# Kernel tuning notes

Hardware: AMD Instinct MI355X
Metric: run time of the kernel (lower is better)

Reference implementation:

```python
import jax, jax.numpy as jnp
import numpy as np

B, H, S, D = 2, 16, 2048, 64


def setup_inputs() -> dict:
    key = jax.random.key(0)
    kq, kk, kv = jax.random.split(key, 3)
    Q = jax.random.normal(kq, (B, H, S, D), dtype=jnp.float32)
    K = jax.random.normal(kk, (B, H, S, D), dtype=jnp.float32)
    V = jax.random.normal(kv, (B, H, S, D), dtype=jnp.float32)
    # causal mask, broadcastable over batch/heads; True = attend
    mask = jnp.tril(jnp.ones((S, S), dtype=bool))[None, None, :, :]
    return {"Q": Q, "K": K, "V": V, "mask": mask}


def reference(Q, K, V, mask):
    d_k = Q.shape[-1]
    # [b,h,s_q,s_k] scores
    scores = jnp.einsum("bhqd,bhkd->bhqk", Q, K) / jnp.sqrt(jnp.float32(d_k))
    scores = jnp.where(mask, scores, -jnp.inf)
    attn = jax.nn.softmax(scores, axis=-1)
    out = jnp.einsum("bhqk,bhkd->bhqd", attn, V)
    return out
```

## Files before the change

kernel.cpp:

```cpp
#include <hip/hip_runtime.h>

#define SDIM 2048
#define DDIM 64
#define BHN  32

using f32x4  = __attribute__((ext_vector_type(4))) float;
using f32x16 = __attribute__((ext_vector_type(16))) float;
using bf16x8 = __attribute__((ext_vector_type(8))) __bf16;
using s16x8  = __attribute__((ext_vector_type(8))) short;

union FragU { s16x8 s; bf16x8 b; uint4 u4; };
union US8   { unsigned short u[8]; uint4 v; };
union PW    { __bf16 h[2]; unsigned int u; };

__device__ __forceinline__ unsigned short f2bf(float f) {
    unsigned int u = __builtin_bit_cast(unsigned int, f);
    u += 0x7fffu + ((u >> 16) & 1u);
    return (unsigned short)(u >> 16);
}

__device__ __forceinline__ unsigned int packbf(float a, float b) {
    PW w; w.h[0] = (__bf16)a; w.h[1] = (__bf16)b; return w.u;
}

__device__ __forceinline__ float fexp2(float x) { return __builtin_amdgcn_exp2f(x); }

__device__ __forceinline__ void gload16(const void* g, void* l) {
    __builtin_amdgcn_global_load_lds(
        (const __attribute__((address_space(1))) void*)g,
        (__attribute__((address_space(3))) void*)l, 16, 0, 0);
}

__global__ __launch_bounds__(256) void conv_fused_kernel(
    const float* __restrict__ K, const float* __restrict__ V,
    unsigned short* __restrict__ Kb, unsigned short* __restrict__ Vt)
{
    const int s0 = blockIdx.x * 64;
    const int bh = blockIdx.y;
    const int t  = threadIdx.x;

    {
        const size_t off = ((size_t)bh * SDIM + s0) * DDIM;
        const float4* src = (const float4*)(K + off);
        float4 a = src[t*4+0], b = src[t*4+1], c = src[t*4+2], d = src[t*4+3];
        US8 o0, o1;
        o0.u[0]=f2bf(a.x); o0.u[1]=f2bf(a.y); o0.u[2]=f2bf(a.z); o0.u[3]=f2bf(a.w);
        o0.u[4]=f2bf(b.x); o0.u[5]=f2bf(b.y); o0.u[6]=f2bf(b.z); o0.u[7]=f2bf(b.w);
        o1.u[0]=f2bf(c.x); o1.u[1]=f2bf(c.y); o1.u[2]=f2bf(c.z); o1.u[3]=f2bf(c.w);
        o1.u[4]=f2bf(d.x); o1.u[5]=f2bf(d.y); o1.u[6]=f2bf(d.z); o1.u[7]=f2bf(d.w);
        *(uint4*)(Kb + off + t*16)     = o0.v;
        *(uint4*)(Kb + off + t*16 + 8) = o1.v;
    }

    __shared__ unsigned short T[64][66];
    {
        const int r = t >> 2, seg = t & 3;
        const float* src = V + ((size_t)bh * SDIM + s0 + r) * DDIM + seg * 16;
        float4 f0 = ((const float4*)src)[0];
        float4 f1 = ((const float4*)src)[1];
        float4 f2 = ((const float4*)src)[2];
        float4 f3 = ((const float4*)src)[3];
        float vv[16] = { f0.x, f0.y, f0.z, f0.w, f1.x, f1.y, f1.z, f1.w,
                         f2.x, f2.y, f2.z, f2.w, f3.x, f3.y, f3.z, f3.w };
        #pragma unroll
        for (int j = 0; j < 16; ++j) T[r][seg * 16 + j] = f2bf(vv[j]);
    }
    __syncthreads();
    {
        const int d = t >> 2, q = t & 3;
        US8 w0, w1;
        #pragma unroll
        for (int j = 0; j < 8; ++j) { w0.u[j] = T[q * 16 + j][d]; w1.u[j] = T[q * 16 + 8 + j][d]; }
        unsigned short* dst = Vt + ((size_t)bh * DDIM + d) * SDIM + s0 + q * 16;
        *(uint4*)dst       = w0.v;
        *(uint4*)(dst + 8) = w1.v;
    }
}

#define M_FIX 12.0f

__device__ __forceinline__ void compute32(
    const unsigned char* __restrict__ Kt, const unsigned char* __restrict__ Vt,
    const FragU* __restrict__ qf, f32x16& o0, f32x16& o1, f32x16& lacc,
    int q_lane, int q0w, int kt64, int l31, int hi)
{
    const int swz = (l31 & 7) << 4;
    const int cb  = hi * 16;

    f32x16 s0 = {}, s1 = {};
    __builtin_amdgcn_s_setprio(1);
    #pragma unroll
    for (int kc = 0; kc < 4; ++kc) {
        FragU k0f, k1f;
        k0f.u4 = *(const uint4*)&Kt[ l31       * 128 + ((kc * 32 + cb) ^ swz)];
        k1f.u4 = *(const uint4*)&Kt[(l31 + 32) * 128 + ((kc * 32 + cb) ^ swz)];
        s0 = __builtin_amdgcn_mfma_f32_32x32x16_bf16(k0f.b, qf[kc].b, s0, 0, 0, 0);
        s1 = __builtin_amdgcn_mfma_f32_32x32x16_bf16(k1f.b, qf[kc].b, s1, 0, 0, 0);
    }
    __builtin_amdgcn_s_setprio(0);

    if (kt64 + 63 > q0w) {
        #pragma unroll
        for (int r = 0; r < 16; ++r) {
            const int kl = (r & 3) + 8 * (r >> 2) + 4 * hi;
            if (kt64 + kl      > q_lane) s0[r] = -1e30f;
            if (kt64 + 32 + kl > q_lane) s1[r] = -1e30f;
        }
    }

    #pragma unroll
    for (int r = 0; r < 16; ++r) { s0[r] = fexp2(s0[r] - M_FIX); s1[r] = fexp2(s1[r] - M_FIX); }
    #pragma unroll
    for (int r = 0; r < 16; ++r) lacc[r] += s0[r] + s1[r];

    FragU pa[4];
    const bool lo = (hi == 0);
    #pragma unroll
    for (int h = 0; h < 2; ++h) {
        #pragma unroll
        for (int sub = 0; sub < 2; ++sub) {
            const int e = sub * 8;
            unsigned int a0, a1, b0, b1;
            if (h == 0) {
                a0 = packbf(s0[e+0], s0[e+1]); a1 = packbf(s0[e+2], s0[e+3]);
                b0 = packbf(s0[e+4], s0[e+5]); b1 = packbf(s0[e+6], s0[e+7]);
            } else {
                a0 = packbf(s1[e+0], s1[e+1]); a1 = packbf(s1[e+2], s1[e+3]);
                b0 = packbf(s1[e+4], s1[e+5]); b1 = packbf(s1[e+6], s1[e+7]);
            }
            const unsigned int send0 = lo ? b0 : a0;
            const unsigned int send1 = lo ? b1 : a1;
            const unsigned int t0 = (unsigned int)__shfl_xor((int)send0, 32, 64);
            const unsigned int t1 = (unsigned int)__shfl_xor((int)send1, 32, 64);
            FragU f;
            f.u4.x = lo ? a0 : t0;
            f.u4.y = lo ? a1 : t1;
            f.u4.z = lo ? t0 : b0;
            f.u4.w = lo ? t1 : b1;
            pa[h * 2 + sub] = f;
        }
    }

    __builtin_amdgcn_s_setprio(1);
    #pragma unroll
    for (int kc = 0; kc < 4; ++kc) {
        FragU v0f, v1f;
        v0f.u4 = *(const uint4*)&Vt[ l31       * 128 + ((kc * 32 + cb) ^ swz)];
        v1f.u4 = *(const uint4*)&Vt[(l31 + 32) * 128 + ((kc * 32 + cb) ^ swz)];
        o0 = __builtin_amdgcn_mfma_f32_32x32x16_bf16(v0f.b, pa[kc].b, o0, 0, 0, 0);
        o1 = __builtin_amdgcn_mfma_f32_32x32x16_bf16(v1f.b, pa[kc].b, o1, 0, 0, 0);
    }
    __builtin_amdgcn_s_setprio(0);
}

__global__ __launch_bounds__(256, 2) void attn_fwd_v17(
    const float* __restrict__ Q, const unsigned short* __restrict__ Kbf,
    const unsigned short* __restrict__ Vtb, float* __restrict__ O)
{
    const int x   = blockIdx.x;
    const int bh  = blockIdx.y;
    const int qtB = 31 - x;
    const int qtA = x;
    const int nB  = 32 - x;
    const int tid  = threadIdx.x;
    const int wid  = tid >> 6;
    const int wg   = wid & 1;
    const int gid  = wid >> 1;
    const int lane = tid & 63;
    const int l31  = lane & 31;
    const int hi   = lane >> 5;

    __shared__ unsigned char Sta[4][16384];
    __shared__ float Ml[2][2][64];

    const size_t base = (size_t)bh * SDIM * DDIM;
    const int q0B = qtB * 64 + wg * 32;
    const int q0A = qtA * 64 + wg * 32;
    const int qBl = q0B + l31, qAl = q0A + l31;

    const float qs = 0.125f * 1.44269504088896f;
    FragU qfA[4], qfB[4];
    #pragma unroll
    for (int kc = 0; kc < 4; ++kc) {
        const int d0 = kc * 16 + hi * 8;
        const float* pA = Q + base + (size_t)qAl * DDIM + d0;
        const float* pB = Q + base + (size_t)qBl * DDIM + d0;
        float4 xa = ((const float4*)pA)[0], ya = ((const float4*)pA)[1];
        float4 xb = ((const float4*)pB)[0], yb = ((const float4*)pB)[1];
        qfA[kc].u4 = make_uint4(packbf(xa.x*qs, xa.y*qs), packbf(xa.z*qs, xa.w*qs),
                                packbf(ya.x*qs, ya.y*qs), packbf(ya.z*qs, ya.w*qs));
        qfB[kc].u4 = make_uint4(packbf(xb.x*qs, xb.y*qs), packbf(xb.z*qs, xb.w*qs),
                                packbf(yb.x*qs, yb.y*qs), packbf(yb.z*qs, yb.w*qs));
    }

    f32x16 oA0 = {}, oA1 = {}, laccA = {};
    f32x16 oB0 = {}, oB1 = {}, laccB = {};

    const char* Vg = (const char*)(Vtb + (size_t)bh * DDIM * SDIM);
    auto stage = [&](int k0, int pb) {
        const char* Kt = (const char*)(Kbf + ((size_t)bh * SDIM + (size_t)k0) * DDIM);
        unsigned char* buf = &Sta[gid * 2 + pb][0];
        #pragma unroll
        for (int c = 0; c < 4; ++c) {
            const int lb = wg * 4096 + c * 1024;
            const int db = lb + lane * 16;
            const int sw = ((db >> 7) & 7) << 4;
            gload16(Kt + (db ^ sw), buf + lb);
            const int d  = db >> 7;
            const int wo = (db & 127) ^ sw;
            gload16(Vg + (size_t)d * (SDIM * 2) + (size_t)k0 * 2 + wo, buf + 8192 + lb);
        }
    };

    const int ubase = gid * 17;
    const int cnt   = gid ? 16 : 17;
    auto unit_k0 = [&](int u) { return ((u < nB) ? u : u - nB) * 64; };
    stage(unit_k0(ubase), 0);
    int pb = 0;
    for (int i = 0; i < 17; ++i) {
        __syncthreads();
        if (i + 1 < cnt) stage(unit_k0(ubase + i + 1), pb ^ 1);
        if (i < cnt) {
            const int u = ubase + i;
            const unsigned char* Kb_ = &Sta[gid * 2 + pb][0];
            const unsigned char* Vb_ = &Sta[gid * 2 + pb][8192];
            if (u < nB) {
                const int kt64 = u * 64;
                if (kt64 <= q0B + 31)
                    compute32(Kb_, Vb_, qfB, oB0, oB1, laccB, qBl, q0B, kt64, l31, hi);
            } else {
                const int kt64 = (u - nB) * 64;
                if (kt64 <= q0A + 31)
                    compute32(Kb_, Vb_, qfA, oA0, oA1, laccA, qAl, q0A, kt64, l31, hi);
            }
        }
        pb ^= 1;
    }

    float lB = ((laccB[0]+laccB[1])+(laccB[2]+laccB[3])) + ((laccB[4]+laccB[5])+(laccB[6]+laccB[7]))
             + ((laccB[8]+laccB[9])+(laccB[10]+laccB[11])) + ((laccB[12]+laccB[13])+(laccB[14]+laccB[15]));
    lB += __shfl_xor(lB, 32, 64);
    float lA = ((laccA[0]+laccA[1])+(laccA[2]+laccA[3])) + ((laccA[4]+laccA[5])+(laccA[6]+laccA[7]))
             + ((laccA[8]+laccA[9])+(laccA[10]+laccA[11])) + ((laccA[12]+laccA[13])+(laccA[14]+laccA[15]));
    lA += __shfl_xor(lA, 32, 64);

    float* ObB = (float*)&Sta[0][0];
    float* ObA = (float*)&Sta[1][0];
    const int ib = wg * 64 + lane;

    __syncthreads();
    if (gid == 1) {
        Ml[0][wg][lane] = lB;
        Ml[1][wg][lane] = lA;
        #pragma unroll
        for (int j = 0; j < 16; ++j) {
            ObB[ j       * 128 + ib] = oB0[j];
            ObB[(j + 16) * 128 + ib] = oB1[j];
            ObA[ j       * 128 + ib] = oA0[j];
            ObA[(j + 16) * 128 + ib] = oA1[j];
        }
    }
    __syncthreads();
    if (gid == 0) {
        const float invB = 1.f / (lB + Ml[0][wg][lane]);
        const float invA = 1.f / (lA + Ml[1][wg][lane]);
        #pragma unroll
        for (int mq = 0; mq < 4; ++mq) {
            const int dm = mq * 8 + hi * 4;
            float4 w;
            w.x = (oB0[4*mq+0] + ObB[(4*mq+0)*128 + ib]) * invB;
            w.y = (oB0[4*mq+1] + ObB[(4*mq+1)*128 + ib]) * invB;
            w.z = (oB0[4*mq+2] + ObB[(4*mq+2)*128 + ib]) * invB;
            w.w = (oB0[4*mq+3] + ObB[(4*mq+3)*128 + ib]) * invB;
            *(float4*)(O + base + (size_t)qBl * DDIM + dm) = w;
            w.x = (oB1[4*mq+0] + ObB[(16+4*mq+0)*128 + ib]) * invB;
            w.y = (oB1[4*mq+1] + ObB[(16+4*mq+1)*128 + ib]) * invB;
            w.z = (oB1[4*mq+2] + ObB[(16+4*mq+2)*128 + ib]) * invB;
            w.w = (oB1[4*mq+3] + ObB[(16+4*mq+3)*128 + ib]) * invB;
            *(float4*)(O + base + (size_t)qBl * DDIM + 32 + dm) = w;
            w.x = (oA0[4*mq+0] + ObA[(4*mq+0)*128 + ib]) * invA;
            w.y = (oA0[4*mq+1] + ObA[(4*mq+1)*128 + ib]) * invA;
            w.z = (oA0[4*mq+2] + ObA[(4*mq+2)*128 + ib]) * invA;
            w.w = (oA0[4*mq+3] + ObA[(4*mq+3)*128 + ib]) * invA;
            *(float4*)(O + base + (size_t)qAl * DDIM + dm) = w;
            w.x = (oA1[4*mq+0] + ObA[(16+4*mq+0)*128 + ib]) * invA;
            w.y = (oA1[4*mq+1] + ObA[(16+4*mq+1)*128 + ib]) * invA;
            w.z = (oA1[4*mq+2] + ObA[(16+4*mq+2)*128 + ib]) * invA;
            w.w = (oA1[4*mq+3] + ObA[(16+4*mq+3)*128 + ib]) * invA;
            *(float4*)(O + base + (size_t)qAl * DDIM + 32 + dm) = w;
        }
    }
}

extern "C" void kernel_launch(void* const* d_in, const int* in_sizes, int n_in,
                              void* d_out, int out_size, void* d_ws, size_t ws_size,
                              hipStream_t stream) {
    const float* Q = (const float*)d_in[0];
    const float* K = (const float*)d_in[1];
    const float* V = (const float*)d_in[2];
    float* O = (float*)d_out;

    const size_t tensor_elems = (size_t)BHN * SDIM * DDIM;
    unsigned short* Kb = (unsigned short*)d_ws;
    unsigned short* Vt = Kb + tensor_elems;

    conv_fused_kernel<<<dim3(SDIM / 64, BHN), dim3(256), 0, stream>>>(K, V, Kb, Vt);
    attn_fwd_v17<<<dim3(16, BHN), dim3(256), 0, stream>>>(Q, Kb, Vt, O);
}
```

Before: 55.73 us.

## Read K/V fragments directly from global memory instead of LDS staging

Removes the double-buffered global_load_lds staging of K and V tiles and the per-iteration block barriers, and has each wave load MFMA fragments straight from global/L2. Shared memory is now only the output-reduction buffers, so launch bounds are raised to 4 blocks per CU to gain occupancy. The trade-off is that loads are no longer shared across the waves of a block and fragment loads now see global latency directly, with no explicit prefetch to hide it.

```diff
diff --git a/kernel.cpp b/kernel.cpp
--- a/kernel.cpp
+++ b/kernel.cpp
@@ -24,12 +24,6 @@
 }
 
 __device__ __forceinline__ float fexp2(float x) { return __builtin_amdgcn_exp2f(x); }
-
-__device__ __forceinline__ void gload16(const void* g, void* l) {
-    __builtin_amdgcn_global_load_lds(
-        (const __attribute__((address_space(1))) void*)g,
-        (__attribute__((address_space(3))) void*)l, 16, 0, 0);
-}
 
 __global__ __launch_bounds__(256) void conv_fused_kernel(
     const float* __restrict__ K, const float* __restrict__ V,
@@ -80,20 +74,20 @@
 #define M_FIX 12.0f
 
 __device__ __forceinline__ void compute32(
-    const unsigned char* __restrict__ Kt, const unsigned char* __restrict__ Vt,
+    const char* __restrict__ Kbyte, const char* __restrict__ Vbyte,
     const FragU* __restrict__ qf, f32x16& o0, f32x16& o1, f32x16& lacc,
     int q_lane, int q0w, int kt64, int l31, int hi)
 {
-    const int swz = (l31 & 7) << 4;
-    const int cb  = hi * 16;
-
+    const int cb = hi * 16;
+
+    const char* pK = Kbyte + (size_t)(kt64 + l31) * 128 + cb;
     f32x16 s0 = {}, s1 = {};
     __builtin_amdgcn_s_setprio(1);
     #pragma unroll
     for (int kc = 0; kc < 4; ++kc) {
         FragU k0f, k1f;
-        k0f.u4 = *(const uint4*)&Kt[ l31       * 128 + ((kc * 32 + cb) ^ swz)];
-        k1f.u4 = *(const uint4*)&Kt[(l31 + 32) * 128 + ((kc * 32 + cb) ^ swz)];
+        k0f.u4 = *(const uint4*)(pK + kc * 32);
+        k1f.u4 = *(const uint4*)(pK + 4096 + kc * 32);
         s0 = __builtin_amdgcn_mfma_f32_32x32x16_bf16(k0f.b, qf[kc].b, s0, 0, 0, 0);
         s1 = __builtin_amdgcn_mfma_f32_32x32x16_bf16(k1f.b, qf[kc].b, s1, 0, 0, 0);
     }
@@ -141,19 +135,20 @@
         }
     }
 
+    const char* pV = Vbyte + (size_t)l31 * 4096 + (size_t)kt64 * 2 + cb;
     __builtin_amdgcn_s_setprio(1);
     #pragma unroll
     for (int kc = 0; kc < 4; ++kc) {
         FragU v0f, v1f;
-        v0f.u4 = *(const uint4*)&Vt[ l31       * 128 + ((kc * 32 + cb) ^ swz)];
-        v1f.u4 = *(const uint4*)&Vt[(l31 + 32) * 128 + ((kc * 32 + cb) ^ swz)];
+        v0f.u4 = *(const uint4*)(pV + kc * 32);
+        v1f.u4 = *(const uint4*)(pV + 32 * 4096 + kc * 32);
         o0 = __builtin_amdgcn_mfma_f32_32x32x16_bf16(v0f.b, pa[kc].b, o0, 0, 0, 0);
         o1 = __builtin_amdgcn_mfma_f32_32x32x16_bf16(v1f.b, pa[kc].b, o1, 0, 0, 0);
     }
     __builtin_amdgcn_s_setprio(0);
 }
 
-__global__ __launch_bounds__(256, 2) void attn_fwd_v17(
+__global__ __launch_bounds__(256, 4) void attn_fwd_v18(
     const float* __restrict__ Q, const unsigned short* __restrict__ Kbf,
     const unsigned short* __restrict__ Vtb, float* __restrict__ O)
 {
@@ -170,7 +165,8 @@
     const int l31  = lane & 31;
     const int hi   = lane >> 5;
 
-    __shared__ unsigned char Sta[4][16384];
+    __shared__ float ObB[32 * 128];
+    __shared__ float ObA[32 * 128];
     __shared__ float Ml[2][2][64];
 
     const size_t base = (size_t)bh * SDIM * DDIM;
@@ -196,45 +192,22 @@
     f32x16 oA0 = {}, oA1 = {}, laccA = {};
     f32x16 oB0 = {}, oB1 = {}, laccB = {};
 
-    const char* Vg = (const char*)(Vtb + (size_t)bh * DDIM * SDIM);
-    auto stage = [&](int k0, int pb) {
-        const char* Kt = (const char*)(Kbf + ((size_t)bh * SDIM + (size_t)k0) * DDIM);
-        unsigned char* buf = &Sta[gid * 2 + pb][0];
-        #pragma unroll
-        for (int c = 0; c < 4; ++c) {
-            const int lb = wg * 4096 + c * 1024;
-            const int db = lb + lane * 16;
-            const int sw = ((db >> 7) & 7) << 4;
-            gload16(Kt + (db ^ sw), buf + lb);
-            const int d  = db >> 7;
-            const int wo = (db & 127) ^ sw;
-            gload16(Vg + (size_t)d * (SDIM * 2) + (size_t)k0 * 2 + wo, buf + 8192 + lb);
-        }
-    };
+    const char* Kbyte = (const char*)(Kbf + base);
+    const char* Vbyte = (const char*)(Vtb + (size_t)bh * DDIM * SDIM);
 
     const int ubase = gid * 17;
     const int cnt   = gid ? 16 : 17;
-    auto unit_k0 = [&](int u) { return ((u < nB) ? u : u - nB) * 64; };
-    stage(unit_k0(ubase), 0);
-    int pb = 0;
-    for (int i = 0; i < 17; ++i) {
-        __syncthreads();
-        if (i + 1 < cnt) stage(unit_k0(ubase + i + 1), pb ^ 1);
-        if (i < cnt) {
-            const int u = ubase + i;
-            const unsigned char* Kb_ = &Sta[gid * 2 + pb][0];
-            const unsigned char* Vb_ = &Sta[gid * 2 + pb][8192];
-            if (u < nB) {
-                const int kt64 = u * 64;
-                if (kt64 <= q0B + 31)
-                    compute32(Kb_, Vb_, qfB, oB0, oB1, laccB, qBl, q0B, kt64, l31, hi);
-            } else {
-                const int kt64 = (u - nB) * 64;
-                if (kt64 <= q0A + 31)
-                    compute32(Kb_, Vb_, qfA, oA0, oA1, laccA, qAl, q0A, kt64, l31, hi);
-            }
-        }
-        pb ^= 1;
+    for (int i = 0; i < cnt; ++i) {
+        const int u = ubase + i;
+        if (u < nB) {
+            const int kt64 = u * 64;
+            if (kt64 <= q0B + 31)
+                compute32(Kbyte, Vbyte, qfB, oB0, oB1, laccB, qBl, q0B, kt64, l31, hi);
+        } else {
+            const int kt64 = (u - nB) * 64;
+            if (kt64 <= q0A + 31)
+                compute32(Kbyte, Vbyte, qfA, oA0, oA1, laccA, qAl, q0A, kt64, l31, hi);
+        }
     }
 
     float lB = ((laccB[0]+laccB[1])+(laccB[2]+laccB[3])) + ((laccB[4]+laccB[5])+(laccB[6]+laccB[7]))
@@ -244,8 +217,6 @@
              + ((laccA[8]+laccA[9])+(laccA[10]+laccA[11])) + ((laccA[12]+laccA[13])+(laccA[14]+laccA[15]));
     lA += __shfl_xor(lA, 32, 64);
 
-    float* ObB = (float*)&Sta[0][0];
-    float* ObA = (float*)&Sta[1][0];
     const int ib = wg * 64 + lane;
 
     __syncthreads();
@@ -305,5 +276,5 @@
     unsigned short* Vt = Kb + tensor_elems;
 
     conv_fused_kernel<<<dim3(SDIM / 64, BHN), dim3(256), 0, stream>>>(K, V, Kb, Vt);
-    attn_fwd_v17<<<dim3(16, BHN), dim3(256), 0, stream>>>(Q, Kb, Vt, O);
-}
+    attn_fwd_v18<<<dim3(16, BHN), dim3(256), 0, stream>>>(Q, Kb, Vt, O);
+}
```

New measurement: 213.1 us. +282.4%, slower.
